# Optimization experiments

Hardware: AMD Instinct MI355X
Metric: run time of the kernel (lower is better)

The kernel has to match this reference:

```python
import jax, jax.numpy as jnp
import numpy as np


def _lstm(x, Wih, Whh, bih, bhh):
    # x: (T, B, F); Wih: (4H, F); Whh: (4H, H); torch gate order i, f, g, o
    T, B, _ = x.shape
    H = Whh.shape[1]
    # precompute input projections for all timesteps (one big GEMM)
    xg = jnp.einsum('tbf,gf->tbg', x, Wih) + bih + bhh  # (T, B, 4H)

    def step(carry, gx):
        h, c = carry
        g = gx + h @ Whh.T  # (B, 4H)
        i, f, gg, o = jnp.split(g, 4, axis=-1)
        i = jax.nn.sigmoid(i)
        f = jax.nn.sigmoid(f)
        gg = jnp.tanh(gg)
        o = jax.nn.sigmoid(o)
        c = f * c + i * gg
        h = o * jnp.tanh(c)
        return (h, c), h

    h0 = jnp.zeros((B, H), x.dtype)
    (_, _), out = jax.lax.scan(step, (h0, h0), xg)
    return out  # (T, B, H)


def setup_inputs() -> dict:
    key = jax.random.key(0)
    ks = jax.random.split(key, 20)
    T, B, F = 1024, 512, 32
    H1, H2, H3 = 32, 8, 8  # lstm1 hidden=32, lstm2 hidden=8, lstm3 hidden=out_features=8
    p = 0.25
    s = 0.1  # weight init scale

    def mk_mask(k, h):
        keep = (jax.random.uniform(k, (B, h)) > p).astype(jnp.float32)
        return keep / (1.0 - p)

    return {
        'x': jax.random.normal(ks[0], (T, B, F), jnp.float32),
        'W_ih1': jax.random.normal(ks[1], (4 * H1, F)) * s,
        'W_hh1': jax.random.normal(ks[2], (4 * H1, H1)) * s,
        'b_ih1': jax.random.normal(ks[3], (4 * H1,)) * s,
        'b_hh1': jax.random.normal(ks[4], (4 * H1,)) * s,
        'W_ih2': jax.random.normal(ks[5], (4 * H2, H1)) * s,
        'W_hh2': jax.random.normal(ks[6], (4 * H2, H2)) * s,
        'b_ih2': jax.random.normal(ks[7], (4 * H2,)) * s,
        'b_hh2': jax.random.normal(ks[8], (4 * H2,)) * s,
        'W_ih3': jax.random.normal(ks[9], (4 * H3, H2)) * s,
        'W_hh3': jax.random.normal(ks[10], (4 * H3, H3)) * s,
        'b_ih3': jax.random.normal(ks[11], (4 * H3,)) * s,
        'b_hh3': jax.random.normal(ks[12], (4 * H3,)) * s,
        'mask1': mk_mask(ks[13], H1),
        'mask2': mk_mask(ks[14], H2),
        'mask3': mk_mask(ks[15], H3),
    }


def reference(x, W_ih1, W_hh1, b_ih1, b_hh1,
              W_ih2, W_hh2, b_ih2, b_hh2,
              W_ih3, W_hh3, b_ih3, b_hh3,
              mask1, mask2, mask3):
    # Locked (variational) output dropout: one mask per sequence, broadcast over time.
    out = _lstm(x, W_ih1, W_hh1, b_ih1, b_hh1) * mask1[None, :, :]
    out = _lstm(out, W_ih2, W_hh2, b_ih2, b_hh2) * mask2[None, :, :]
    out = _lstm(out, W_ih3, W_hh3, b_ih3, b_hh3) * mask3[None, :, :]
    return out  # (T, B, out_features)
```

## Files before the change

kernel.cpp:

```cpp
#include <hip/hip_runtime.h>


constexpr int T = 1024, B = 512, F = 32;
constexpr int H1 = 32, H2 = 8, H3 = 8;
constexpr int G1 = 4 * H1;
constexpr int HR = 128;
constexpr int XR = 64;
constexpr int OUT_STRIDE = B * H3;

#define PIN(v) asm volatile("" : "+v"(v))

#if __has_builtin(__builtin_amdgcn_rcpf)
#define RCPF(x) __builtin_amdgcn_rcpf(x)
#else
#define RCPF(x) (1.0f / (x))
#endif
#if __has_builtin(__builtin_amdgcn_exp2f)
#define EXP2F(x) __builtin_amdgcn_exp2f(x)
#else
#define EXP2F(x) exp2f(x)
#endif

#define SIG_CM (-1.4426950408889634f)

__device__ __forceinline__ float act_f(float v, float cm, float ka, float kb) {
    return fmaf(ka, RCPF(1.0f + EXP2F(v * cm)), kb);
}
__device__ __forceinline__ float tanh_fast(float v) {
    return fmaf(2.0f, RCPF(1.0f + EXP2F(v * (2.0f * SIG_CM))), -1.0f);
}

#define FMA4(ACC, WARR, VEC, BASE)                                             \
    ACC = fmaf(WARR[(BASE) + 0], VEC.x, ACC);                                  \
    ACC = fmaf(WARR[(BASE) + 1], VEC.y, ACC);                                  \
    ACC = fmaf(WARR[(BASE) + 2], VEC.z, ACC);                                  \
    ACC = fmaf(WARR[(BASE) + 3], VEC.w, ACC);

#define LDS_ACQ(p)    __hip_atomic_load((p), __ATOMIC_ACQUIRE, __HIP_MEMORY_SCOPE_WORKGROUP)
#define LDS_REL(p, v) __hip_atomic_store((p), (v), __ATOMIC_RELEASE, __HIP_MEMORY_SCOPE_WORKGROUP)
#define SPIN_UNTIL(EXPR)                                                       \
    do {                                                                       \
        int _g = 0;                                                            \
        while (!(EXPR)) {                                                      \
            __builtin_amdgcn_s_sleep(2);                                       \
            if (++_g > (1 << 22)) break;                                       \
        }                                                                      \
    } while (0)

__global__ __launch_bounds__(192, 1) void lstm3_fused_kernel(
    const float* __restrict__ x,
    const float* __restrict__ Wih1, const float* __restrict__ Whh1,
    const float* __restrict__ bih1, const float* __restrict__ bhh1,
    const float* __restrict__ Wih2, const float* __restrict__ Whh2,
    const float* __restrict__ bih2, const float* __restrict__ bhh2,
    const float* __restrict__ Wih3, const float* __restrict__ Whh3,
    const float* __restrict__ bih3, const float* __restrict__ bhh3,
    const float* __restrict__ mask1, const float* __restrict__ mask2,
    const float* __restrict__ mask3,
    float* __restrict__ out)
{
    const int tid = threadIdx.x;
    const int lane = tid & 63;
    const int wid = tid >> 6;
    const int b = blockIdx.x;

    __shared__ __align__(16) float h1ring[HR][H1];
    __shared__ __align__(16) float xgring[XR][G1];
    __shared__ __align__(16) float xstage[32][F];
    __shared__ __align__(16) float sh23[2][16];
    __shared__ int prog0, prog1, prog2;

    if (tid == 0) { prog0 = 0; prog1 = 0; prog2 = 0; }
    if (wid == 0 && lane < H1) h1ring[HR - 1][lane] = 0.f;
    if (wid == 1 && lane < 16) { sh23[0][lane] = 0.f; sh23[1][lane] = 0.f; }
    __syncthreads();

    if (wid == 2) {
        float wi0[F], wi1[F];
#pragma unroll
        for (int k = 0; k < F; ++k) wi0[k] = Wih1[lane * F + k];
#pragma unroll
        for (int k = 0; k < F; ++k) wi1[k] = Wih1[(lane + 64) * F + k];
        const float bias0 = bih1[lane] + bhh1[lane];
        const float bias1 = bih1[lane + 64] + bhh1[lane + 64];
#pragma unroll
        for (int k = 0; k < F; ++k) { PIN(wi0[k]); PIN(wi1[k]); }

        const float4* x4 = (const float4*)x;
        float4* xr4 = (float4*)xstage;
        const int ttq = lane >> 3, ffq = lane & 7;

        float4 sA = x4[(size_t)(0 + ttq) * 4096 + b * 8 + ffq];
        float4 sB = x4[(size_t)(8 + ttq) * 4096 + b * 8 + ffq];
        xr4[(ttq & 31) * 8 + ffq] = sA;
        xr4[((8 + ttq) & 31) * 8 + ffq] = sB;
        sA = x4[(size_t)(16 + ttq) * 4096 + b * 8 + ffq];
        sB = x4[(size_t)(24 + ttq) * 4096 + b * 8 + ffq];

        for (int t = 0; t < T; ++t) {
            if ((t & 15) == 0) {
                const int need = t - 40;
                if (need > 0) SPIN_UNTIL(LDS_ACQ(&prog0) >= need);
                const int wt = t + 16;
                if (wt < T) {
                    xr4[((wt + ttq) & 31) * 8 + ffq] = sA;
                    xr4[((wt + 8 + ttq) & 31) * 8 + ffq] = sB;
                    const int lt = t + 32;
                    if (lt < T) {
                        sA = x4[(size_t)(lt + ttq) * 4096 + b * 8 + ffq];
                        sB = x4[(size_t)(lt + 8 + ttq) * 4096 + b * 8 + ffq];
                    }
                }
            }
            const float4* xp = (const float4*)xstage[t & 31];
            float aA = bias0, aB = 0.f, cA = bias1, cB = 0.f;
#pragma unroll
            for (int q = 0; q < 8; q += 2) {
                const float4 v0 = xp[q], v1 = xp[q + 1];
                FMA4(aA, wi0, v0, q * 4); FMA4(aB, wi0, v1, q * 4 + 4);
                FMA4(cA, wi1, v0, q * 4); FMA4(cB, wi1, v1, q * 4 + 4);
            }
            xgring[t & (XR - 1)][lane] = aA + aB;
            xgring[t & (XR - 1)][lane + 64] = cA + cB;
            if ((t & 15) == 15) LDS_REL(&prog2, t + 1);
        }
    } else if (wid == 0) {
        float w0[H1], w1[H1];
#pragma unroll
        for (int k = 0; k < H1; ++k) w0[k] = Whh1[lane * H1 + k];
#pragma unroll
        for (int k = 0; k < H1; ++k) w1[k] = Whh1[(lane + 64) * H1 + k];
#pragma unroll
        for (int k = 0; k < H1; ++k) { PIN(w0[k]); PIN(w1[k]); }
        const float cm1 = (lane < 32) ? 2.0f * SIG_CM : SIG_CM;
        const float ka1 = (lane < 32) ? 2.0f : 1.0f;
        const float kb1 = (lane < 32) ? -1.0f : 0.0f;
        float c1 = 0.f;

        SPIN_UNTIL(LDS_ACQ(&prog2) >= ((34 < T) ? 34 : T));
        float pa = xgring[0][lane], pb = xgring[0][lane + 64];
        float na = xgring[1][lane], nb = xgring[1][lane + 64];

        for (int i = 0; i < T; ++i) {
            if ((i & 31) == 0 && i) {
                int tgt = i + 34; if (tgt > T) tgt = T;
                SPIN_UNTIL(LDS_ACQ(&prog2) >= tgt);
            }
            if ((i & 63) == 0 && i >= 64)
                SPIN_UNTIL(LDS_ACQ(&prog1) >= i - 48);

            const float4* h1p = (const float4*)h1ring[(i - 1) & (HR - 1)];
            float aA = 0.f, aB = 0.f, aC = 0.f, aD = 0.f;
            float bA = 0.f, bB = 0.f, bC = 0.f, bD = 0.f;
            {
                const float4 v0 = h1p[0], v1 = h1p[1], v2 = h1p[2], v3 = h1p[3];
                FMA4(aA, w0, v0, 0);  FMA4(aB, w0, v1, 4);
                FMA4(aC, w0, v2, 8);  FMA4(aD, w0, v3, 12);
                FMA4(bA, w1, v0, 0);  FMA4(bB, w1, v1, 4);
                FMA4(bC, w1, v2, 8);  FMA4(bD, w1, v3, 12);
            }
            {
                const float4 v4 = h1p[4], v5 = h1p[5], v6 = h1p[6], v7 = h1p[7];
                FMA4(aA, w0, v4, 16); FMA4(aB, w0, v5, 20);
                FMA4(aC, w0, v6, 24); FMA4(aD, w0, v7, 28);
                FMA4(bA, w1, v4, 16); FMA4(bB, w1, v5, 20);
                FMA4(bC, w1, v6, 24); FMA4(bD, w1, v7, 28);
            }
            const float a0 = pa + ((aA + aB) + (aC + aD));
            const float a1 = pb + ((bA + bB) + (bC + bD));
            const float g0 = act_f(a0, SIG_CM, 1.0f, 0.0f);
            const float g1 = act_f(a1, cm1, ka1, kb1);
            pa = na; pb = nb;
            {
                int tn = i + 2; if (tn > T - 1) tn = T - 1;
                na = xgring[tn & (XR - 1)][lane];
                nb = xgring[tn & (XR - 1)][lane + 64];
            }
            const float f_ = __shfl_xor(g0, 32);
            const float o_ = __shfl_xor(g1, 32);
            c1 = fmaf(f_, c1, g0 * g1);
            const float h1v = o_ * tanh_fast(c1);
            if (lane < H1) h1ring[i & (HR - 1)][lane] = h1v;
            if ((i & 7) == 7) LDS_REL(&prog0, i + 1);
        }
    } else {
        float wreg[48];
        float biasX, m3;
        const int r = lane & 31;
        const bool lower = (lane < 32);
        if (lower) {
#pragma unroll
            for (int k = 0; k < H1; ++k) wreg[k] = Wih2[r * H1 + k] * mask1[b * H1 + k];
#pragma unroll
            for (int k = 0; k < H2; ++k) wreg[32 + k] = Whh2[r * H2 + k];
#pragma unroll
            for (int k = 0; k < H3; ++k) wreg[40 + k] = 0.0f;
            biasX = bih2[r] + bhh2[r];
        } else {
#pragma unroll
            for (int k = 0; k < H1; ++k) wreg[k] = 0.0f;
#pragma unroll
            for (int k = 0; k < H2; ++k) wreg[32 + k] = Wih3[r * H2 + k] * mask2[b * H2 + k];
#pragma unroll
            for (int k = 0; k < H3; ++k) wreg[40 + k] = Whh3[r * H3 + k];
            biasX = bih3[r] + bhh3[r];
        }
        const int sec = r >> 3;
        const float cmX = (sec == 2) ? 2.0f * SIG_CM : SIG_CM;
        const float kaX = (sec == 2) ? 2.0f : 1.0f;
        const float kbX = (sec == 2) ? -1.0f : 0.0f;
        m3 = mask3[b * H3 + (lane & 7)];
        const int thresh = lower ? 1 : 2;
        const int gbase = (lane & 32) + (lane & 7);
#pragma unroll
        for (int k = 0; k < 48; ++k) PIN(wreg[k]);

        float c23 = 0.f;
        for (int i = 0; i <= T + 1; ++i) {
            if ((i & 7) == 0) {
                int tgt = i + 7; if (tgt > T) tgt = T;
                SPIN_UNTIL(LDS_ACQ(&prog0) >= tgt);
            }
            const int par = i & 1;
            const float4* h1p = (const float4*)h1ring[(i - 1) & (HR - 1)];
            const float4* up = (const float4*)sh23[par ^ 1];
            float s0 = 0.f, s1 = 0.f, s2 = 0.f, s3 = 0.f;
            {
                const float4 v0 = h1p[0], v1 = h1p[1], v2 = h1p[2];
                FMA4(s0, wreg, v0, 0);  FMA4(s0, wreg, v1, 4);  FMA4(s0, wreg, v2, 8);
            }
            {
                const float4 v3 = h1p[3], v4 = h1p[4], v5 = h1p[5];
                FMA4(s1, wreg, v3, 12); FMA4(s1, wreg, v4, 16); FMA4(s1, wreg, v5, 20);
            }
            {
                const float4 v6 = h1p[6], v7 = h1p[7], u0 = up[0];
                FMA4(s2, wreg, v6, 24); FMA4(s2, wreg, v7, 28); FMA4(s2, wreg, u0, 32);
            }
            {
                const float4 u1 = up[1], u2 = up[2], u3 = up[3];
                FMA4(s3, wreg, u1, 36); FMA4(s3, wreg, u2, 40); FMA4(s3, wreg, u3, 44);
            }
            const float a23 = biasX + (s0 + s1) + (s2 + s3);
            const float rv = act_f(a23, cmX, kaX, kbX);
            const float gi = __shfl(rv, gbase);
            const float gf = __shfl(rv, gbase + 8);
            const float gg = __shfl(rv, gbase + 16);
            const float go = __shfl(rv, gbase + 24);
            c23 = (i >= thresh) ? fmaf(gf, c23, gi * gg) : 0.0f;
            const float hnew = go * tanh_fast(c23);
            if (i >= 2 && (lane & 56) == 32)
                out[(size_t)(i - 2) * OUT_STRIDE + b * H3 + (lane & 7)] = hnew * m3;
            if ((lane & 24) == 0)
                sh23[par][(lane & 7) | ((lane & 32) >> 2)] = hnew;
            if ((i & 15) == 15) LDS_REL(&prog1, i + 1);
        }
    }
}

extern "C" void kernel_launch(void* const* d_in, const int* in_sizes, int n_in,
                              void* d_out, int out_size, void* d_ws, size_t ws_size,
                              hipStream_t stream) {
    (void)in_sizes; (void)n_in; (void)out_size; (void)d_ws; (void)ws_size;
    const float* x     = (const float*)d_in[0];
    const float* Wih1  = (const float*)d_in[1];
    const float* Whh1  = (const float*)d_in[2];
    const float* bih1  = (const float*)d_in[3];
    const float* bhh1  = (const float*)d_in[4];
    const float* Wih2  = (const float*)d_in[5];
    const float* Whh2  = (const float*)d_in[6];
    const float* bih2  = (const float*)d_in[7];
    const float* bhh2  = (const float*)d_in[8];
    const float* Wih3  = (const float*)d_in[9];
    const float* Whh3  = (const float*)d_in[10];
    const float* bih3  = (const float*)d_in[11];
    const float* bhh3  = (const float*)d_in[12];
    const float* mask1 = (const float*)d_in[13];
    const float* mask2 = (const float*)d_in[14];
    const float* mask3 = (const float*)d_in[15];
    float* out = (float*)d_out;

    lstm3_fused_kernel<<<dim3(B), dim3(192), 0, stream>>>(
        x, Wih1, Whh1, bih1, bhh1,
        Wih2, Whh2, bih2, bhh2,
        Wih3, Whh3, bih3, bhh3,
        mask1, mask2, mask3, out);
}
```

Before: 585.4 us.

## Use packed FP32 FMAs, permlane32 swap, and batched bpermutes in LSTM kernel

Converts the per-step dot products in all three wavefronts (input projection, layer-1 recurrence, layers 2/3) to two-wide float vectors so the compiler can emit packed FP32 FMA instructions, halving the FMA instruction count on the serial recurrence chain. Layer 1 replaces the two xor-32 shuffles with permlane32_swap when the builtin is available. Layers 2/3 issue four ds_bpermute gathers in inline asm with a single wait instead of four separate shuffles. This adds reliance on compiler vectorization and inline asm that bypasses the compiler's scheduling of waitcnts.

```diff
diff --git a/kernel.cpp b/kernel.cpp
--- a/kernel.cpp
+++ b/kernel.cpp
@@ -7,6 +7,9 @@
 constexpr int HR = 128;
 constexpr int XR = 64;
 constexpr int OUT_STRIDE = B * H3;
+
+typedef float f32x2 __attribute__((ext_vector_type(2)));
+typedef unsigned int u32x2 __attribute__((ext_vector_type(2)));
 
 #define PIN(v) asm volatile("" : "+v"(v))
 
@@ -21,6 +24,12 @@
 #define EXP2F(x) exp2f(x)
 #endif
 
+#if __has_builtin(__builtin_amdgcn_permlane32_swap)
+#define HAVE_PLSWAP 1
+#else
+#define HAVE_PLSWAP 0
+#endif
+
 #define SIG_CM (-1.4426950408889634f)
 
 __device__ __forceinline__ float act_f(float v, float cm, float ka, float kb) {
@@ -30,11 +39,9 @@
     return fmaf(2.0f, RCPF(1.0f + EXP2F(v * (2.0f * SIG_CM))), -1.0f);
 }
 
-#define FMA4(ACC, WARR, VEC, BASE)                                             \
-    ACC = fmaf(WARR[(BASE) + 0], VEC.x, ACC);                                  \
-    ACC = fmaf(WARR[(BASE) + 1], VEC.y, ACC);                                  \
-    ACC = fmaf(WARR[(BASE) + 2], VEC.z, ACC);                                  \
-    ACC = fmaf(WARR[(BASE) + 3], VEC.w, ACC);
+__device__ __forceinline__ void pkfma(f32x2& acc, f32x2 a, f32x2 b) {
+    acc += a * b;
+}
 
 #define LDS_ACQ(p)    __hip_atomic_load((p), __ATOMIC_ACQUIRE, __HIP_MEMORY_SCOPE_WORKGROUP)
 #define LDS_REL(p, v) __hip_atomic_store((p), (v), __ATOMIC_RELEASE, __HIP_MEMORY_SCOPE_WORKGROUP)
@@ -76,15 +83,16 @@
     __syncthreads();
 
     if (wid == 2) {
-        float wi0[F], wi1[F];
-#pragma unroll
-        for (int k = 0; k < F; ++k) wi0[k] = Wih1[lane * F + k];
-#pragma unroll
-        for (int k = 0; k < F; ++k) wi1[k] = Wih1[(lane + 64) * F + k];
+        f32x2 wi0[16], wi1[16];
+#pragma unroll
+        for (int k = 0; k < 16; ++k) {
+            wi0[k] = f32x2{Wih1[lane * F + 2 * k], Wih1[lane * F + 2 * k + 1]};
+            wi1[k] = f32x2{Wih1[(lane + 64) * F + 2 * k], Wih1[(lane + 64) * F + 2 * k + 1]};
+        }
         const float bias0 = bih1[lane] + bhh1[lane];
         const float bias1 = bih1[lane + 64] + bhh1[lane + 64];
 #pragma unroll
-        for (int k = 0; k < F; ++k) { PIN(wi0[k]); PIN(wi1[k]); }
+        for (int k = 0; k < 16; ++k) { PIN(wi0[k]); PIN(wi1[k]); }
 
         const float4* x4 = (const float4*)x;
         float4* xr4 = (float4*)xstage;
@@ -113,25 +121,29 @@
                 }
             }
             const float4* xp = (const float4*)xstage[t & 31];
-            float aA = bias0, aB = 0.f, cA = bias1, cB = 0.f;
-#pragma unroll
-            for (int q = 0; q < 8; q += 2) {
-                const float4 v0 = xp[q], v1 = xp[q + 1];
-                FMA4(aA, wi0, v0, q * 4); FMA4(aB, wi0, v1, q * 4 + 4);
-                FMA4(cA, wi1, v0, q * 4); FMA4(cB, wi1, v1, q * 4 + 4);
-            }
-            xgring[t & (XR - 1)][lane] = aA + aB;
-            xgring[t & (XR - 1)][lane + 64] = cA + cB;
+            f32x2 aA = f32x2{bias0, 0.f}, aB = f32x2{0.f, 0.f};
+            f32x2 cA = f32x2{bias1, 0.f}, cB = f32x2{0.f, 0.f};
+#pragma unroll
+            for (int q = 0; q < 8; ++q) {
+                const float4 v = xp[q];
+                const f32x2 lo = f32x2{v.x, v.y}, hi = f32x2{v.z, v.w};
+                pkfma(aA, wi0[2 * q], lo); pkfma(aB, wi0[2 * q + 1], hi);
+                pkfma(cA, wi1[2 * q], lo); pkfma(cB, wi1[2 * q + 1], hi);
+            }
+            const f32x2 sa = aA + aB, sc = cA + cB;
+            xgring[t & (XR - 1)][lane] = sa.x + sa.y;
+            xgring[t & (XR - 1)][lane + 64] = sc.x + sc.y;
             if ((t & 15) == 15) LDS_REL(&prog2, t + 1);
         }
     } else if (wid == 0) {
-        float w0[H1], w1[H1];
-#pragma unroll
-        for (int k = 0; k < H1; ++k) w0[k] = Whh1[lane * H1 + k];
-#pragma unroll
-        for (int k = 0; k < H1; ++k) w1[k] = Whh1[(lane + 64) * H1 + k];
-#pragma unroll
-        for (int k = 0; k < H1; ++k) { PIN(w0[k]); PIN(w1[k]); }
+        f32x2 w0[16], w1[16];
+#pragma unroll
+        for (int k = 0; k < 16; ++k) {
+            w0[k] = f32x2{Whh1[lane * H1 + 2 * k], Whh1[lane * H1 + 2 * k + 1]};
+            w1[k] = f32x2{Whh1[(lane + 64) * H1 + 2 * k], Whh1[(lane + 64) * H1 + 2 * k + 1]};
+        }
+#pragma unroll
+        for (int k = 0; k < 16; ++k) { PIN(w0[k]); PIN(w1[k]); }
         const float cm1 = (lane < 32) ? 2.0f * SIG_CM : SIG_CM;
         const float ka1 = (lane < 32) ? 2.0f : 1.0f;
         const float kb1 = (lane < 32) ? -1.0f : 0.0f;
@@ -150,24 +162,18 @@
                 SPIN_UNTIL(LDS_ACQ(&prog1) >= i - 48);
 
             const float4* h1p = (const float4*)h1ring[(i - 1) & (HR - 1)];
-            float aA = 0.f, aB = 0.f, aC = 0.f, aD = 0.f;
-            float bA = 0.f, bB = 0.f, bC = 0.f, bD = 0.f;
-            {
-                const float4 v0 = h1p[0], v1 = h1p[1], v2 = h1p[2], v3 = h1p[3];
-                FMA4(aA, w0, v0, 0);  FMA4(aB, w0, v1, 4);
-                FMA4(aC, w0, v2, 8);  FMA4(aD, w0, v3, 12);
-                FMA4(bA, w1, v0, 0);  FMA4(bB, w1, v1, 4);
-                FMA4(bC, w1, v2, 8);  FMA4(bD, w1, v3, 12);
-            }
-            {
-                const float4 v4 = h1p[4], v5 = h1p[5], v6 = h1p[6], v7 = h1p[7];
-                FMA4(aA, w0, v4, 16); FMA4(aB, w0, v5, 20);
-                FMA4(aC, w0, v6, 24); FMA4(aD, w0, v7, 28);
-                FMA4(bA, w1, v4, 16); FMA4(bB, w1, v5, 20);
-                FMA4(bC, w1, v6, 24); FMA4(bD, w1, v7, 28);
-            }
-            const float a0 = pa + ((aA + aB) + (aC + aD));
-            const float a1 = pb + ((bA + bB) + (bC + bD));
+            f32x2 A0 = f32x2{0.f, 0.f}, A1 = f32x2{0.f, 0.f};
+            f32x2 B0 = f32x2{0.f, 0.f}, B1 = f32x2{0.f, 0.f};
+#pragma unroll
+            for (int q = 0; q < 8; ++q) {
+                const float4 v = h1p[q];
+                const f32x2 lo = f32x2{v.x, v.y}, hi = f32x2{v.z, v.w};
+                pkfma(A0, w0[2 * q], lo); pkfma(A1, w0[2 * q + 1], hi);
+                pkfma(B0, w1[2 * q], lo); pkfma(B1, w1[2 * q + 1], hi);
+            }
+            const f32x2 SA = A0 + A1, SB = B0 + B1;
+            const float a0 = pa + (SA.x + SA.y);
+            const float a1 = pb + (SB.x + SB.y);
             const float g0 = act_f(a0, SIG_CM, 1.0f, 0.0f);
             const float g1 = act_f(a1, cm1, ka1, kb1);
             pa = na; pb = nb;
@@ -176,33 +182,53 @@
                 na = xgring[tn & (XR - 1)][lane];
                 nb = xgring[tn & (XR - 1)][lane + 64];
             }
-            const float f_ = __shfl_xor(g0, 32);
-            const float o_ = __shfl_xor(g1, 32);
-            c1 = fmaf(f_, c1, g0 * g1);
-            const float h1v = o_ * tanh_fast(c1);
+            float h1v;
+#if HAVE_PLSWAP
+            const u32x2 pif = __builtin_amdgcn_permlane32_swap(
+                __float_as_uint(g0), __float_as_uint(g0), false, false);
+            const u32x2 pgo = __builtin_amdgcn_permlane32_swap(
+                __float_as_uint(g1), __float_as_uint(g1), false, false);
+            const float iv = __uint_as_float(pif.x);
+            const float fv = __uint_as_float(pif.y);
+            const float gv = __uint_as_float(pgo.x);
+            const float ov = __uint_as_float(pgo.y);
+            c1 = fmaf(fv, c1, iv * gv);
+            h1v = ov * tanh_fast(c1);
+#else
+            const float fv = __shfl_xor(g0, 32);
+            const float ov = __shfl_xor(g1, 32);
+            c1 = fmaf(fv, c1, g0 * g1);
+            h1v = ov * tanh_fast(c1);
+#endif
             if (lane < H1) h1ring[i & (HR - 1)][lane] = h1v;
             if ((i & 7) == 7) LDS_REL(&prog0, i + 1);
         }
     } else {
-        float wreg[48];
+        f32x2 wp[24];
         float biasX, m3;
         const int r = lane & 31;
         const bool lower = (lane < 32);
         if (lower) {
 #pragma unroll
-            for (int k = 0; k < H1; ++k) wreg[k] = Wih2[r * H1 + k] * mask1[b * H1 + k];
-#pragma unroll
-            for (int k = 0; k < H2; ++k) wreg[32 + k] = Whh2[r * H2 + k];
-#pragma unroll
-            for (int k = 0; k < H3; ++k) wreg[40 + k] = 0.0f;
+            for (int k = 0; k < 16; ++k)
+                wp[k] = f32x2{Wih2[r * H1 + 2 * k] * mask1[b * H1 + 2 * k],
+                              Wih2[r * H1 + 2 * k + 1] * mask1[b * H1 + 2 * k + 1]};
+#pragma unroll
+            for (int k = 0; k < 4; ++k)
+                wp[16 + k] = f32x2{Whh2[r * H2 + 2 * k], Whh2[r * H2 + 2 * k + 1]};
+#pragma unroll
+            for (int k = 0; k < 4; ++k) wp[20 + k] = f32x2{0.f, 0.f};
             biasX = bih2[r] + bhh2[r];
         } else {
 #pragma unroll
-            for (int k = 0; k < H1; ++k) wreg[k] = 0.0f;
-#pragma unroll
-            for (int k = 0; k < H2; ++k) wreg[32 + k] = Wih3[r * H2 + k] * mask2[b * H2 + k];
-#pragma unroll
-            for (int k = 0; k < H3; ++k) wreg[40 + k] = Whh3[r * H3 + k];
+            for (int k = 0; k < 16; ++k) wp[k] = f32x2{0.f, 0.f};
+#pragma unroll
+            for (int k = 0; k < 4; ++k)
+                wp[16 + k] = f32x2{Wih3[r * H2 + 2 * k] * mask2[b * H2 + 2 * k],
+                                   Wih3[r * H2 + 2 * k + 1] * mask2[b * H2 + 2 * k + 1]};
+#pragma unroll
+            for (int k = 0; k < 4; ++k)
+                wp[20 + k] = f32x2{Whh3[r * H3 + 2 * k], Whh3[r * H3 + 2 * k + 1]};
             biasX = bih3[r] + bhh3[r];
         }
         const int sec = r >> 3;
@@ -212,8 +238,10 @@
         m3 = mask3[b * H3 + (lane & 7)];
         const int thresh = lower ? 1 : 2;
         const int gbase = (lane & 32) + (lane & 7);
-#pragma unroll
-        for (int k = 0; k < 48; ++k) PIN(wreg[k]);
+        const int bx0 = 4 * (gbase + 0),  bx1 = 4 * (gbase + 8);
+        const int bx2 = 4 * (gbase + 16), bx3 = 4 * (gbase + 24);
+#pragma unroll
+        for (int k = 0; k < 24; ++k) PIN(wp[k]);
 
         float c23 = 0.f;
         for (int i = 0; i <= T + 1; ++i) {
@@ -224,29 +252,39 @@
             const int par = i & 1;
             const float4* h1p = (const float4*)h1ring[(i - 1) & (HR - 1)];
             const float4* up = (const float4*)sh23[par ^ 1];
-            float s0 = 0.f, s1 = 0.f, s2 = 0.f, s3 = 0.f;
+            f32x2 s0 = f32x2{0.f, 0.f}, s1 = f32x2{0.f, 0.f};
+            f32x2 s2 = f32x2{0.f, 0.f}, s3 = f32x2{0.f, 0.f};
+#pragma unroll
+            for (int q = 0; q < 4; ++q) {
+                const float4 v = h1p[q], w = h1p[q + 4];
+                pkfma(s0, wp[2 * q], f32x2{v.x, v.y});
+                pkfma(s0, wp[2 * q + 1], f32x2{v.z, v.w});
+                pkfma(s1, wp[8 + 2 * q], f32x2{w.x, w.y});
+                pkfma(s1, wp[8 + 2 * q + 1], f32x2{w.z, w.w});
+            }
             {
-                const float4 v0 = h1p[0], v1 = h1p[1], v2 = h1p[2];
-                FMA4(s0, wreg, v0, 0);  FMA4(s0, wreg, v1, 4);  FMA4(s0, wreg, v2, 8);
-            }
-            {
-                const float4 v3 = h1p[3], v4 = h1p[4], v5 = h1p[5];
-                FMA4(s1, wreg, v3, 12); FMA4(s1, wreg, v4, 16); FMA4(s1, wreg, v5, 20);
-            }
-            {
-                const float4 v6 = h1p[6], v7 = h1p[7], u0 = up[0];
-                FMA4(s2, wreg, v6, 24); FMA4(s2, wreg, v7, 28); FMA4(s2, wreg, u0, 32);
-            }
-            {
-                const float4 u1 = up[1], u2 = up[2], u3 = up[3];
-                FMA4(s3, wreg, u1, 36); FMA4(s3, wreg, u2, 40); FMA4(s3, wreg, u3, 44);
-            }
-            const float a23 = biasX + (s0 + s1) + (s2 + s3);
+                const float4 u0 = up[0], u1 = up[1], u2 = up[2], u3 = up[3];
+                pkfma(s2, wp[16], f32x2{u0.x, u0.y});
+                pkfma(s2, wp[17], f32x2{u0.z, u0.w});
+                pkfma(s2, wp[18], f32x2{u1.x, u1.y});
+                pkfma(s2, wp[19], f32x2{u1.z, u1.w});
+                pkfma(s3, wp[20], f32x2{u2.x, u2.y});
+                pkfma(s3, wp[21], f32x2{u2.z, u2.w});
+                pkfma(s3, wp[22], f32x2{u3.x, u3.y});
+                pkfma(s3, wp[23], f32x2{u3.z, u3.w});
+            }
+            const f32x2 st = (s0 + s1) + (s2 + s3);
+            const float a23 = biasX + st.x + st.y;
             const float rv = act_f(a23, cmX, kaX, kbX);
-            const float gi = __shfl(rv, gbase);
-            const float gf = __shfl(rv, gbase + 8);
-            const float gg = __shfl(rv, gbase + 16);
-            const float go = __shfl(rv, gbase + 24);
+            float gi, gf, gg, go;
+            asm volatile(
+                "ds_bpermute_b32 %0, %4, %8\n\t"
+                "ds_bpermute_b32 %1, %5, %8\n\t"
+                "ds_bpermute_b32 %2, %6, %8\n\t"
+                "ds_bpermute_b32 %3, %7, %8\n\t"
+                "s_waitcnt lgkmcnt(0)"
+                : "=&v"(gi), "=&v"(gf), "=&v"(gg), "=&v"(go)
+                : "v"(bx0), "v"(bx1), "v"(bx2), "v"(bx3), "v"(rv));
             c23 = (i >= thresh) ? fmaf(gf, c23, gi * gg) : 0.0f;
             const float hnew = go * tanh_fast(c23);
             if (i >= 2 && (lane & 56) == 32)
```

Result: faster. 539.2 us (-7.9%).
